# Optimization experiments

Hardware: AMD Instinct MI355X
Metric: run time of the kernel (lower is better)

Reference implementation:

```python
import jax, jax.numpy as jnp
import numpy as np

N = 100000
E = 1600000

def setup_inputs() -> dict:
    key = jax.random.key(0)
    ks = jax.random.split(key, 8)
    x = jax.random.normal(ks[0], (N, 512), dtype=jnp.float32)
    edge_index = jax.random.randint(ks[1], (2, E), 0, N, dtype=jnp.int32)
    W1 = jax.random.normal(ks[2], (512, 64), dtype=jnp.float32) * (1.0 / np.sqrt(512))
    b1 = jnp.zeros((64,), dtype=jnp.float32)
    W2 = jax.random.normal(ks[3], (64, 32), dtype=jnp.float32) * (1.0 / np.sqrt(64))
    b2 = jnp.zeros((32,), dtype=jnp.float32)
    W3 = jax.random.normal(ks[4], (32, 4), dtype=jnp.float32) * (1.0 / np.sqrt(32))
    b3 = jnp.zeros((4,), dtype=jnp.float32)
    return {"x": x, "edge_index": edge_index, "W1": W1, "b1": b1,
            "W2": W2, "b2": b2, "W3": W3, "b3": b3}


def _gcn_norm(edge_index, n):
    # Add self-loops (fill_value=1), symmetric deg^{-1/2} normalization (PyG gcn_norm).
    loop = jnp.arange(n, dtype=edge_index.dtype)
    src = jnp.concatenate([edge_index[0], loop])
    dst = jnp.concatenate([edge_index[1], loop])
    w = jnp.ones((src.shape[0],), dtype=jnp.float32)
    deg = jax.ops.segment_sum(w, dst, num_segments=n)
    dinv = jnp.where(deg > 0, jax.lax.rsqrt(deg), 0.0)
    norm = dinv[src] * w * dinv[dst]
    return src, dst, norm


def _gcn_conv(x, W, b, src, dst, norm, n):
    h = x @ W                      # dense transform first (PyG GCNConv order)
    msg = h[src] * norm[:, None]   # gather + edge scaling
    out = jax.ops.segment_sum(msg, dst, num_segments=n)  # scatter-add aggregate
    return out + b


def reference(x, edge_index, W1, b1, W2, b2, W3, b3):
    n = x.shape[0]
    src, dst, norm = _gcn_norm(edge_index, n)  # cached=True: shared across layers
    h = jax.nn.relu(_gcn_conv(x, W1, b1, src, dst, norm, n))
    # dropout p=0.2 is identity in eval mode
    h = jax.nn.relu(_gcn_conv(h, W2, b2, src, dst, norm, n))
    # dropout p=0.4 is identity in eval mode
    out = _gcn_conv(h, W3, b3, src, dst, norm, n)
    return out
```

## Files before the change

### kernel.cpp

```cpp
#include <hip/hip_runtime.h>


typedef __attribute__((ext_vector_type(8))) short short8;
typedef __attribute__((ext_vector_type(4))) float floatx4;

#define NBUK_MAX 512
#define SC_EDGES 8192
#define CB_MAXE 6144
#define HIST_EDGES 8192

__device__ __forceinline__ unsigned f2bf_bits(float f) {
    unsigned u = __float_as_uint(f);
    return (u + 0x7fffu + ((u >> 16) & 1u)) >> 16;
}
__device__ __forceinline__ float bf_bits2f(unsigned b) {
    return __uint_as_float(b << 16);
}

__global__ __launch_bounds__(256) void zero_i32(int* p, int n) {
    int i = blockIdx.x * 256 + threadIdx.x;
    if (i < n) p[i] = 0;
}

__global__ __launch_bounds__(512) void bucket_hist(const int* __restrict__ dst,
                                                   int* __restrict__ buckcnt,
                                                   int e, int shift, int nbuk) {
    __shared__ int hist[NBUK_MAX];
    int t = threadIdx.x;
    for (int i = t; i < nbuk; i += 512) hist[i] = 0;
    __syncthreads();
    long long base = (long long)blockIdx.x * HIST_EDGES;
#pragma unroll
    for (int j = 0; j < HIST_EDGES / 512; j++) {
        long long i = base + j * 512 + t;
        if (i < e) atomicAdd(&hist[dst[i] >> shift], 1);
    }
    __syncthreads();
    for (int i = t; i < nbuk; i += 512)
        if (hist[i] > 0) atomicAdd(&buckcnt[i], hist[i]);
}

__global__ __launch_bounds__(512) void bucket_scan(const int* __restrict__ buckcnt,
                                                   int* __restrict__ boff,
                                                   int* __restrict__ buckfill,
                                                   int* __restrict__ rowptr,
                                                   int nbuk, int n, int e) {
    __shared__ int sc[512];
    int t = threadIdx.x;
    int v = (t < nbuk) ? buckcnt[t] : 0;
    sc[t] = v;
    __syncthreads();
    for (int off = 1; off < 512; off <<= 1) {
        int u = (t >= off) ? sc[t - off] : 0;
        __syncthreads();
        sc[t] += u;
        __syncthreads();
    }
    int excl = sc[t] - v;
    if (t < nbuk) {
        boff[t] = excl;
        buckfill[t] = excl;
    }
    if (t == 0) {
        boff[nbuk] = e;
        rowptr[n] = e;
    }
}

__global__ __launch_bounds__(512) void bucket_scatter(const int* __restrict__ src,
                                                      const int* __restrict__ dst,
                                                      int* __restrict__ buckfill,
                                                      unsigned* __restrict__ colpack,
                                                      int e, int shift, int nbuk) {
    __shared__ int cnt[NBUK_MAX];
    __shared__ int baseG[NBUK_MAX];
    int t = threadIdx.x;
    for (int i = t; i < nbuk; i += 512) cnt[i] = 0;
    __syncthreads();
    long long base = (long long)blockIdx.x * SC_EDGES;
    unsigned wreg[16];
    int breg[16];
    unsigned lomask = (1u << shift) - 1u;
#pragma unroll
    for (int j = 0; j < 16; j++) {
        long long i = base + j * 512 + t;
        bool ok = (i < e);
        int d = ok ? dst[i] : 0;
        int s = ok ? src[i] : 0;
        int b = d >> shift;
        int r = ok ? atomicAdd(&cnt[b], 1) : 0;
        wreg[j] = ((unsigned)s << shift) | ((unsigned)d & lomask);
        breg[j] = ok ? ((b << 16) | r) : -1;
    }
    __syncthreads();
    for (int i = t; i < nbuk; i += 512) {
        int v = cnt[i];
        baseG[i] = (v > 0) ? atomicAdd(&buckfill[i], v) : 0;
    }
    __syncthreads();
#pragma unroll
    for (int j = 0; j < 16; j++) {
        int br = breg[j];
        if (br >= 0) {
            int b = br >> 16, r = br & 0xffff;
            colpack[baseG[b] + r] = wreg[j];
        }
    }
}

__global__ __launch_bounds__(512) void csr_build(const unsigned* __restrict__ colpack,
                                                 const int* __restrict__ boff,
                                                 int* __restrict__ rowptr,
                                                 float* __restrict__ dinv,
                                                 int* __restrict__ colidx,
                                                 int n, int shift) {
    __shared__ int degl[NBUK_MAX];
    __shared__ int lsc[NBUK_MAX];
    int t = threadIdx.x;
    int bn = 1 << shift;
    unsigned lomask = (unsigned)bn - 1u;
    int node0 = blockIdx.x << shift;
    int e0 = boff[blockIdx.x];
    int e1 = boff[blockIdx.x + 1];
    int cnt = e1 - e0;
    if (t < bn) degl[t] = 0;
    __syncthreads();
    unsigned wreg[CB_MAXE / 512];
    int rreg[CB_MAXE / 512];
#pragma unroll
    for (int j = 0; j < CB_MAXE / 512; j++) {
        int k = j * 512 + t;
        bool ok = (k < cnt);
        unsigned w = ok ? colpack[e0 + k] : 0u;
        int dlo = (int)(w & lomask);
        rreg[j] = ok ? atomicAdd(&degl[dlo], 1) : -1;
        wreg[j] = w;
    }
    __syncthreads();
    int v = (t < bn) ? degl[t] : 0;
    lsc[t] = v;
    __syncthreads();
    for (int off = 1; off < 512; off <<= 1) {
        int u = (t >= off) ? lsc[t - off] : 0;
        __syncthreads();
        lsc[t] += u;
        __syncthreads();
    }
    int excl = lsc[t] - v;
    int node = node0 + t;
    if (t < bn && node < n) {
        rowptr[node] = e0 + excl;
        dinv[node] = rsqrtf((float)(v + 1));
    }
    __syncthreads();
    if (t < 512) lsc[t] = excl;
    __syncthreads();
#pragma unroll
    for (int j = 0; j < CB_MAXE / 512; j++) {
        if (rreg[j] >= 0) {
            unsigned w = wreg[j];
            int dlo = (int)(w & lomask);
            colidx[e0 + lsc[dlo] + rreg[j]] = (int)(w >> shift);
        }
    }
}

__global__ __launch_bounds__(256) void w1_split(const float* __restrict__ W1,
                                                short* __restrict__ whi,
                                                short* __restrict__ wlo) {
    int idx = blockIdx.x * 256 + threadIdx.x;
    int k = idx >> 6;
    int nn = idx & 63;
    float v = W1[idx];
    unsigned hb = f2bf_bits(v);
    float lof = v - bf_bits2f(hb);
    unsigned lb = f2bf_bits(lof);
    int kc = k >> 5, rem = k & 31, quad = rem >> 3, j = rem & 7;
    int ct = nn >> 4, l = nn & 15;
    int lane = quad * 16 + l;
    int addr = ((ct * 16 + kc) * 64 + lane) * 8 + j;
    whi[addr] = (short)hb;
    wlo[addr] = (short)lb;
}

__global__ __launch_bounds__(256) void transform1_mfma(const float* __restrict__ x,
                                                       const short* __restrict__ whi,
                                                       const short* __restrict__ wlo,
                                                       const float* __restrict__ dinv,
                                                       float* __restrict__ h1, int n) {
    __shared__ float xs[64 * 36];
    const int t = threadIdx.x;
    const int w = t >> 6;
    const int lane = t & 63;
    const int quad = lane >> 4;
    const int row0 = blockIdx.x * 64;
    const int mrow = w * 16 + (lane & 15);
    floatx4 acc[4] = {{0.f, 0.f, 0.f, 0.f}, {0.f, 0.f, 0.f, 0.f},
                      {0.f, 0.f, 0.f, 0.f}, {0.f, 0.f, 0.f, 0.f}};

    for (int kc = 0; kc < 16; kc++) {
        __syncthreads();
#pragma unroll
        for (int i = 0; i < 2; i++) {
            int c = t + i * 256;
            int m = c >> 3;
            int koff = (c & 7) << 2;
            int grow = row0 + m;
            float4 v = make_float4(0.f, 0.f, 0.f, 0.f);
            if (grow < n) v = *(const float4*)&x[(size_t)grow * 512 + kc * 32 + koff];
            *(float4*)&xs[m * 36 + koff] = v;
        }
        __syncthreads();
        float a[8];
        *(float4*)&a[0] = *(const float4*)&xs[mrow * 36 + quad * 8];
        *(float4*)&a[4] = *(const float4*)&xs[mrow * 36 + quad * 8 + 4];
        short8 ahi, alo;
#pragma unroll
        for (int j = 0; j < 8; j++) {
            unsigned hb = f2bf_bits(a[j]);
            float lof = a[j] - bf_bits2f(hb);
            unsigned lb = f2bf_bits(lof);
            ahi[j] = (short)hb;
            alo[j] = (short)lb;
        }
        const int base = (kc * 64 + lane) * 8;
#pragma unroll
        for (int ct = 0; ct < 4; ct++) {
            short8 bhi = *(const short8*)&whi[ct * 8192 + base];
            short8 blo = *(const short8*)&wlo[ct * 8192 + base];
            acc[ct] = __builtin_amdgcn_mfma_f32_16x16x32_bf16(ahi, bhi, acc[ct], 0, 0, 0);
            acc[ct] = __builtin_amdgcn_mfma_f32_16x16x32_bf16(alo, bhi, acc[ct], 0, 0, 0);
            acc[ct] = __builtin_amdgcn_mfma_f32_16x16x32_bf16(ahi, blo, acc[ct], 0, 0, 0);
        }
    }
#pragma unroll
    for (int r = 0; r < 4; r++) {
        int grow = row0 + w * 16 + quad * 4 + r;
        if (grow < n) {
            float s = dinv[grow];
#pragma unroll
            for (int ct = 0; ct < 4; ct++) {
                h1[(size_t)grow * 64 + ct * 16 + (lane & 15)] = acc[ct][r] * s;
            }
        }
    }
}

__global__ __launch_bounds__(256) void transform2(const float* __restrict__ g1,
                                                  const float* __restrict__ W2,
                                                  const float* __restrict__ dinv,
                                                  float* __restrict__ h2, int n) {
    __shared__ float rows[32 * 68];
    __shared__ float W2s[64 * 32];
    int t = threadIdx.x;
    int row0 = blockIdx.x * 32;
#pragma unroll
    for (int i = 0; i < 2; i++) {
        int c = t + i * 256;
        int r = c >> 4, k4 = (c & 15) << 2;
        int grow = row0 + r;
        float4 v = make_float4(0.f, 0.f, 0.f, 0.f);
        if (grow < n) v = *(const float4*)&g1[(size_t)grow * 64 + k4];
        *(float4*)&rows[r * 68 + k4] = v;
    }
#pragma unroll
    for (int i = 0; i < 2; i++) {
        int c = t + i * 256;
        *(float4*)&W2s[c * 4] = *(const float4*)&W2[c * 4];
    }
    __syncthreads();
    int lr = t >> 3;
    int c4 = (t & 7) * 4;
    int row = row0 + lr;
    float a0 = 0.f, a1 = 0.f, a2 = 0.f, a3 = 0.f;
#pragma unroll
    for (int k4 = 0; k4 < 64; k4 += 4) {
        float4 a = *(const float4*)&rows[lr * 68 + k4];
        float4 w0 = *(const float4*)&W2s[(k4 + 0) * 32 + c4];
        float4 w1 = *(const float4*)&W2s[(k4 + 1) * 32 + c4];
        float4 w2 = *(const float4*)&W2s[(k4 + 2) * 32 + c4];
        float4 w3 = *(const float4*)&W2s[(k4 + 3) * 32 + c4];
        a0 += a.x * w0.x + a.y * w1.x + a.z * w2.x + a.w * w3.x;
        a1 += a.x * w0.y + a.y * w1.y + a.z * w2.y + a.w * w3.y;
        a2 += a.x * w0.z + a.y * w1.z + a.z * w2.z + a.w * w3.z;
        a3 += a.x * w0.w + a.y * w1.w + a.z * w2.w + a.w * w3.w;
    }
    if (row < n) {
        float s = dinv[row];
        float4 o = make_float4(a0 * s, a1 * s, a2 * s, a3 * s);
        *(float4*)&h2[(size_t)row * 32 + c4] = o;
    }
}

__device__ __forceinline__ void f4acc(float4& a, const float4 b) {
    a.x += b.x; a.y += b.y; a.z += b.z; a.w += b.w;
}
__device__ __forceinline__ void f4shflxor(float4& a, int m) {
    a.x += __shfl_xor(a.x, m);
    a.y += __shfl_xor(a.y, m);
    a.z += __shfl_xor(a.z, m);
    a.w += __shfl_xor(a.w, m);
}

__global__ __launch_bounds__(256) void agg64_wave(const float* __restrict__ h,
                                                  const int* __restrict__ rowptr,
                                                  const int* __restrict__ colidx,
                                                  const float* __restrict__ dinv,
                                                  const float* __restrict__ bias,
                                                  float* __restrict__ out, int n) {
    int node = (blockIdx.x * 256 + threadIdx.x) >> 6;
    if (node >= n) return;
    int lane = threadIdx.x & 63;
    int eslot = lane >> 4;
    int fq = (lane & 15) << 2;
    int r0 = rowptr[node], r1 = rowptr[node + 1];
    float4 z = make_float4(0.f, 0.f, 0.f, 0.f);
    float4 a0 = z, a1 = z, a2 = z, a3 = z;
    if (eslot == 0) a0 = *(const float4*)&h[(size_t)node * 64 + fq];
    int j = r0;
    for (; j + 15 < r1; j += 16) {
        int c0 = colidx[j + eslot];
        int c1 = colidx[j + 4 + eslot];
        int c2 = colidx[j + 8 + eslot];
        int c3 = colidx[j + 12 + eslot];
        f4acc(a0, *(const float4*)&h[(size_t)c0 * 64 + fq]);
        f4acc(a1, *(const float4*)&h[(size_t)c1 * 64 + fq]);
        f4acc(a2, *(const float4*)&h[(size_t)c2 * 64 + fq]);
        f4acc(a3, *(const float4*)&h[(size_t)c3 * 64 + fq]);
    }
    {
        int e0 = j + eslot, e1 = j + 4 + eslot, e2 = j + 8 + eslot, e3 = j + 12 + eslot;
        if (e0 < r1) f4acc(a0, *(const float4*)&h[(size_t)colidx[e0] * 64 + fq]);
        if (e1 < r1) f4acc(a1, *(const float4*)&h[(size_t)colidx[e1] * 64 + fq]);
        if (e2 < r1) f4acc(a2, *(const float4*)&h[(size_t)colidx[e2] * 64 + fq]);
        if (e3 < r1) f4acc(a3, *(const float4*)&h[(size_t)colidx[e3] * 64 + fq]);
    }
    f4acc(a0, a1); f4acc(a2, a3); f4acc(a0, a2);
    f4shflxor(a0, 16);
    f4shflxor(a0, 32);
    if (eslot == 0) {
        float dn = dinv[node];
        float4 b = *(const float4*)&bias[fq];
        float4 v = make_float4(fmaxf(dn * a0.x + b.x, 0.f), fmaxf(dn * a0.y + b.y, 0.f),
                               fmaxf(dn * a0.z + b.z, 0.f), fmaxf(dn * a0.w + b.w, 0.f));
        *(float4*)&out[(size_t)node * 64 + fq] = v;
    }
}

__global__ __launch_bounds__(256) void agg32_t3(const float* __restrict__ h,
                                                const int* __restrict__ rowptr,
                                                const int* __restrict__ colidx,
                                                const float* __restrict__ dinv,
                                                const float* __restrict__ bias,
                                                const float* __restrict__ W3,
                                                float* __restrict__ h3, int n) {
    int node = (blockIdx.x * 256 + threadIdx.x) >> 6;
    if (node >= n) return;
    int lane = threadIdx.x & 63;
    int eslot = lane >> 3;
    int fq = (lane & 7) << 2;
    int r0 = rowptr[node], r1 = rowptr[node + 1];
    float4 z = make_float4(0.f, 0.f, 0.f, 0.f);
    float4 a0 = z, a1 = z;
    if (eslot == 0) a0 = *(const float4*)&h[(size_t)node * 32 + fq];
    int j = r0;
    for (; j + 15 < r1; j += 16) {
        int c0 = colidx[j + eslot];
        int c1 = colidx[j + 8 + eslot];
        f4acc(a0, *(const float4*)&h[(size_t)c0 * 32 + fq]);
        f4acc(a1, *(const float4*)&h[(size_t)c1 * 32 + fq]);
    }
    {
        int e0 = j + eslot, e1 = j + 8 + eslot;
        if (e0 < r1) f4acc(a0, *(const float4*)&h[(size_t)colidx[e0] * 32 + fq]);
        if (e1 < r1) f4acc(a1, *(const float4*)&h[(size_t)colidx[e1] * 32 + fq]);
    }
    f4acc(a0, a1);
    f4shflxor(a0, 8);
    f4shflxor(a0, 16);
    f4shflxor(a0, 32);
    float dn = dinv[node];
    float4 b = *(const float4*)&bias[fq];
    float4 g = make_float4(fmaxf(dn * a0.x + b.x, 0.f), fmaxf(dn * a0.y + b.y, 0.f),
                           fmaxf(dn * a0.z + b.z, 0.f), fmaxf(dn * a0.w + b.w, 0.f));
    float4 w0 = *(const float4*)&W3[(fq + 0) * 4];
    float4 w1 = *(const float4*)&W3[(fq + 1) * 4];
    float4 w2 = *(const float4*)&W3[(fq + 2) * 4];
    float4 w3 = *(const float4*)&W3[(fq + 3) * 4];
    float4 p = make_float4(g.x * w0.x + g.y * w1.x + g.z * w2.x + g.w * w3.x,
                           g.x * w0.y + g.y * w1.y + g.z * w2.y + g.w * w3.y,
                           g.x * w0.z + g.y * w1.z + g.z * w2.z + g.w * w3.z,
                           g.x * w0.w + g.y * w1.w + g.z * w2.w + g.w * w3.w);
    f4shflxor(p, 1);
    f4shflxor(p, 2);
    f4shflxor(p, 4);
    if (lane == 0) {
        *(float4*)&h3[(size_t)node * 4] =
            make_float4(dn * p.x, dn * p.y, dn * p.z, dn * p.w);
    }
}

__global__ __launch_bounds__(256) void agg4_wave(const float* __restrict__ h,
                                                 const int* __restrict__ rowptr,
                                                 const int* __restrict__ colidx,
                                                 const float* __restrict__ dinv,
                                                 const float* __restrict__ bias,
                                                 float* __restrict__ out, int n) {
    int node = (blockIdx.x * 256 + threadIdx.x) >> 6;
    if (node >= n) return;
    int lane = threadIdx.x & 63;
    int eslot = lane >> 2;
    int f = lane & 3;
    int r0 = rowptr[node], r1 = rowptr[node + 1];
    float a0 = (eslot == 0) ? h[(size_t)node * 4 + f] : 0.f;
    float a1 = 0.f;
    int j = r0;
    for (; j + 15 < r1; j += 16) {
        int c = colidx[j + eslot];
        a0 += h[(size_t)c * 4 + f];
    }
    {
        int e = j + eslot;
        if (e < r1) a1 += h[(size_t)colidx[e] * 4 + f];
    }
    float s = a0 + a1;
    s += __shfl_xor(s, 4);
    s += __shfl_xor(s, 8);
    s += __shfl_xor(s, 16);
    s += __shfl_xor(s, 32);
    if (eslot == 0) out[(size_t)node * 4 + f] = dinv[node] * s + bias[f];
}

extern "C" void kernel_launch(void* const* d_in, const int* in_sizes, int n_in,
                              void* d_out, int out_size, void* d_ws, size_t ws_size,
                              hipStream_t stream) {
    const float* x  = (const float*)d_in[0];
    const int*   ei = (const int*)d_in[1];
    const float* W1 = (const float*)d_in[2];
    const float* b1 = (const float*)d_in[3];
    const float* W2 = (const float*)d_in[4];
    const float* b2 = (const float*)d_in[5];
    const float* W3 = (const float*)d_in[6];
    const float* b3 = (const float*)d_in[7];
    const int n = in_sizes[0] / 512;
    const int e = in_sizes[1] / 2;
    const int* src = ei;
    const int* dst = ei + e;
    float* out = (float*)d_out;

    char* p = (char*)d_ws;
    auto alloc = [&](size_t bytes) {
        void* r = (void*)p;
        p += (bytes + 255) & ~(size_t)255;
        return r;
    };
    int*   buckcnt  = (int*)alloc((size_t)NBUK_MAX * 4);
    int*   boff     = (int*)alloc((size_t)(NBUK_MAX + 1) * 4);
    int*   buckfill = (int*)alloc((size_t)NBUK_MAX * 4);
    int*   rowptr   = (int*)alloc((size_t)(n + 1) * 4);
    int*   colidx   = (int*)alloc((size_t)e * 4);
    float* dinv     = (float*)alloc((size_t)n * 4);
    short* whi      = (short*)alloc((size_t)32768 * 2);
    short* wlo      = (short*)alloc((size_t)32768 * 2);
    float* bufA     = (float*)alloc((size_t)n * 64 * 4);
    float* bufB     = (float*)alloc((size_t)n * 64 * 4);
    unsigned* colpack = (unsigned*)bufA;

    int shift = 8;
    while (((n + (1 << shift) - 1) >> shift) > NBUK_MAX) shift++;
    const int nbuk = (n + (1 << shift) - 1) >> shift;

    const int HB = (int)(((long long)e + HIST_EDGES - 1) / HIST_EDGES);
    const int SB = (int)(((long long)e + SC_EDGES - 1) / SC_EDGES);
    const int WPN = (n + 3) / 4;

    zero_i32<<<dim3((nbuk + 255) / 256), dim3(256), 0, stream>>>(buckcnt, nbuk);
    bucket_hist<<<dim3(HB), dim3(512), 0, stream>>>(dst, buckcnt, e, shift, nbuk);
    bucket_scan<<<dim3(1), dim3(512), 0, stream>>>(buckcnt, boff, buckfill, rowptr, nbuk, n, e);
    bucket_scatter<<<dim3(SB), dim3(512), 0, stream>>>(src, dst, buckfill, colpack, e, shift, nbuk);
    csr_build<<<dim3(nbuk), dim3(512), 0, stream>>>(colpack, boff, rowptr, dinv, colidx, n, shift);
    w1_split<<<dim3(128), dim3(256), 0, stream>>>(W1, whi, wlo);

    transform1_mfma<<<dim3((n + 63) / 64), dim3(256), 0, stream>>>(x, whi, wlo, dinv, bufA, n);
    agg64_wave<<<dim3(WPN), dim3(256), 0, stream>>>(bufA, rowptr, colidx, dinv, b1, bufB, n);
    transform2<<<dim3((n + 31) / 32), dim3(256), 0, stream>>>(bufB, W2, dinv, bufA, n);
    agg32_t3<<<dim3(WPN), dim3(256), 0, stream>>>(bufA, rowptr, colidx, dinv, b2, W3, bufB, n);
    agg4_wave<<<dim3(WPN), dim3(256), 0, stream>>>(bufB, rowptr, colidx, dinv, b3, out, n);
}
```

Baseline: 514.1 us.

## Fuse layer-2 transform into layer-1 aggregation and prefetch x tiles

Removes the separate transform2 kernel by applying W2 inside the 64-wide aggregation kernel via wave shuffles and an LDS copy of W2. This avoids writing and re-reading the 64-wide hidden activation. Also restructures transform1 so the next x tile is loaded into registers while the current tile is consumed from LDS. The fused kernel adds per-node shuffle work and a W2 load into LDS per block.

```diff
diff --git a/kernel.cpp b/kernel.cpp
--- a/kernel.cpp
+++ b/kernel.cpp
@@ -195,22 +195,28 @@
     const int quad = lane >> 4;
     const int row0 = blockIdx.x * 64;
     const int mrow = w * 16 + (lane & 15);
+    const int m0 = t >> 3;
+    const int k0 = (t & 7) << 2;
+    const int m1 = m0 + 32;
+    const bool ok0 = (row0 + m0) < n;
+    const bool ok1 = (row0 + m1) < n;
+    const float* xp0 = x + (size_t)(row0 + m0) * 512 + k0;
+    const float* xp1 = x + (size_t)(row0 + m1) * 512 + k0;
+    const float4 z4 = make_float4(0.f, 0.f, 0.f, 0.f);
+    float4 p0 = ok0 ? *(const float4*)xp0 : z4;
+    float4 p1 = ok1 ? *(const float4*)xp1 : z4;
+
     floatx4 acc[4] = {{0.f, 0.f, 0.f, 0.f}, {0.f, 0.f, 0.f, 0.f},
                       {0.f, 0.f, 0.f, 0.f}, {0.f, 0.f, 0.f, 0.f}};
 
     for (int kc = 0; kc < 16; kc++) {
-        __syncthreads();
-#pragma unroll
-        for (int i = 0; i < 2; i++) {
-            int c = t + i * 256;
-            int m = c >> 3;
-            int koff = (c & 7) << 2;
-            int grow = row0 + m;
-            float4 v = make_float4(0.f, 0.f, 0.f, 0.f);
-            if (grow < n) v = *(const float4*)&x[(size_t)grow * 512 + kc * 32 + koff];
-            *(float4*)&xs[m * 36 + koff] = v;
-        }
-        __syncthreads();
+        *(float4*)&xs[m0 * 36 + k0] = p0;
+        *(float4*)&xs[m1 * 36 + k0] = p1;
+        __syncthreads();
+        if (kc < 15) {
+            p0 = ok0 ? *(const float4*)(xp0 + (kc + 1) * 32) : z4;
+            p1 = ok1 ? *(const float4*)(xp1 + (kc + 1) * 32) : z4;
+        }
         float a[8];
         *(float4*)&a[0] = *(const float4*)&xs[mrow * 36 + quad * 8];
         *(float4*)&a[4] = *(const float4*)&xs[mrow * 36 + quad * 8 + 4];
@@ -232,6 +238,7 @@
             acc[ct] = __builtin_amdgcn_mfma_f32_16x16x32_bf16(alo, bhi, acc[ct], 0, 0, 0);
             acc[ct] = __builtin_amdgcn_mfma_f32_16x16x32_bf16(ahi, blo, acc[ct], 0, 0, 0);
         }
+        __syncthreads();
     }
 #pragma unroll
     for (int r = 0; r < 4; r++) {
@@ -243,52 +250,6 @@
                 h1[(size_t)grow * 64 + ct * 16 + (lane & 15)] = acc[ct][r] * s;
             }
         }
-    }
-}
-
-__global__ __launch_bounds__(256) void transform2(const float* __restrict__ g1,
-                                                  const float* __restrict__ W2,
-                                                  const float* __restrict__ dinv,
-                                                  float* __restrict__ h2, int n) {
-    __shared__ float rows[32 * 68];
-    __shared__ float W2s[64 * 32];
-    int t = threadIdx.x;
-    int row0 = blockIdx.x * 32;
-#pragma unroll
-    for (int i = 0; i < 2; i++) {
-        int c = t + i * 256;
-        int r = c >> 4, k4 = (c & 15) << 2;
-        int grow = row0 + r;
-        float4 v = make_float4(0.f, 0.f, 0.f, 0.f);
-        if (grow < n) v = *(const float4*)&g1[(size_t)grow * 64 + k4];
-        *(float4*)&rows[r * 68 + k4] = v;
-    }
-#pragma unroll
-    for (int i = 0; i < 2; i++) {
-        int c = t + i * 256;
-        *(float4*)&W2s[c * 4] = *(const float4*)&W2[c * 4];
-    }
-    __syncthreads();
-    int lr = t >> 3;
-    int c4 = (t & 7) * 4;
-    int row = row0 + lr;
-    float a0 = 0.f, a1 = 0.f, a2 = 0.f, a3 = 0.f;
-#pragma unroll
-    for (int k4 = 0; k4 < 64; k4 += 4) {
-        float4 a = *(const float4*)&rows[lr * 68 + k4];
-        float4 w0 = *(const float4*)&W2s[(k4 + 0) * 32 + c4];
-        float4 w1 = *(const float4*)&W2s[(k4 + 1) * 32 + c4];
-        float4 w2 = *(const float4*)&W2s[(k4 + 2) * 32 + c4];
-        float4 w3 = *(const float4*)&W2s[(k4 + 3) * 32 + c4];
-        a0 += a.x * w0.x + a.y * w1.x + a.z * w2.x + a.w * w3.x;
-        a1 += a.x * w0.y + a.y * w1.y + a.z * w2.y + a.w * w3.y;
-        a2 += a.x * w0.z + a.y * w1.z + a.z * w2.z + a.w * w3.z;
-        a3 += a.x * w0.w + a.y * w1.w + a.z * w2.w + a.w * w3.w;
-    }
-    if (row < n) {
-        float s = dinv[row];
-        float4 o = make_float4(a0 * s, a1 * s, a2 * s, a3 * s);
-        *(float4*)&h2[(size_t)row * 32 + c4] = o;
     }
 }
 
@@ -302,15 +263,24 @@
     a.w += __shfl_xor(a.w, m);
 }
 
-__global__ __launch_bounds__(256) void agg64_wave(const float* __restrict__ h,
-                                                  const int* __restrict__ rowptr,
-                                                  const int* __restrict__ colidx,
-                                                  const float* __restrict__ dinv,
-                                                  const float* __restrict__ bias,
-                                                  float* __restrict__ out, int n) {
-    int node = (blockIdx.x * 256 + threadIdx.x) >> 6;
+__global__ __launch_bounds__(256) void agg64_t2(const float* __restrict__ h,
+                                                const int* __restrict__ rowptr,
+                                                const int* __restrict__ colidx,
+                                                const float* __restrict__ dinv,
+                                                const float* __restrict__ b1,
+                                                const float* __restrict__ W2,
+                                                float* __restrict__ h2, int n) {
+    __shared__ float W2s[64 * 32];
+    int t = threadIdx.x;
+#pragma unroll
+    for (int i = 0; i < 2; i++) {
+        int c = t + i * 256;
+        *(float4*)&W2s[c * 4] = *(const float4*)&W2[c * 4];
+    }
+    __syncthreads();
+    int node = (blockIdx.x * 256 + t) >> 6;
     if (node >= n) return;
-    int lane = threadIdx.x & 63;
+    int lane = t & 63;
     int eslot = lane >> 4;
     int fq = (lane & 15) << 2;
     int r0 = rowptr[node], r1 = rowptr[node + 1];
@@ -338,13 +308,22 @@
     f4acc(a0, a1); f4acc(a2, a3); f4acc(a0, a2);
     f4shflxor(a0, 16);
     f4shflxor(a0, 32);
-    if (eslot == 0) {
-        float dn = dinv[node];
-        float4 b = *(const float4*)&bias[fq];
-        float4 v = make_float4(fmaxf(dn * a0.x + b.x, 0.f), fmaxf(dn * a0.y + b.y, 0.f),
-                               fmaxf(dn * a0.z + b.z, 0.f), fmaxf(dn * a0.w + b.w, 0.f));
-        *(float4*)&out[(size_t)node * 64 + fq] = v;
-    }
+    float dn = dinv[node];
+    float4 bb = *(const float4*)&b1[fq];
+    float4 g = make_float4(fmaxf(dn * a0.x + bb.x, 0.f), fmaxf(dn * a0.y + bb.y, 0.f),
+                           fmaxf(dn * a0.z + bb.z, 0.f), fmaxf(dn * a0.w + bb.w, 0.f));
+    int c = lane & 31;
+    float acc2 = 0.f;
+#pragma unroll
+    for (int kk = 0; kk < 16; kk++) {
+        float gx = __shfl(g.x, kk);
+        float gy = __shfl(g.y, kk);
+        float gz = __shfl(g.z, kk);
+        float gw = __shfl(g.w, kk);
+        acc2 += gx * W2s[(4 * kk + 0) * 32 + c] + gy * W2s[(4 * kk + 1) * 32 + c]
+              + gz * W2s[(4 * kk + 2) * 32 + c] + gw * W2s[(4 * kk + 3) * 32 + c];
+    }
+    if (lane < 32) h2[(size_t)node * 32 + c] = dn * acc2;
 }
 
 __global__ __launch_bounds__(256) void agg32_t3(const float* __restrict__ h,
@@ -482,8 +461,7 @@
     w1_split<<<dim3(128), dim3(256), 0, stream>>>(W1, whi, wlo);
 
     transform1_mfma<<<dim3((n + 63) / 64), dim3(256), 0, stream>>>(x, whi, wlo, dinv, bufA, n);
-    agg64_wave<<<dim3(WPN), dim3(256), 0, stream>>>(bufA, rowptr, colidx, dinv, b1, bufB, n);
-    transform2<<<dim3((n + 31) / 32), dim3(256), 0, stream>>>(bufB, W2, dinv, bufA, n);
-    agg32_t3<<<dim3(WPN), dim3(256), 0, stream>>>(bufA, rowptr, colidx, dinv, b2, W3, bufB, n);
-    agg4_wave<<<dim3(WPN), dim3(256), 0, stream>>>(bufB, rowptr, colidx, dinv, b3, out, n);
-}
+    agg64_t2<<<dim3(WPN), dim3(256), 0, stream>>>(bufA, rowptr, colidx, dinv, b1, W2, bufB, n);
+    agg32_t3<<<dim3(WPN), dim3(256), 0, stream>>>(bufB, rowptr, colidx, dinv, b2, W3, bufA, n);
+    agg4_wave<<<dim3(WPN), dim3(256), 0, stream>>>(bufA, rowptr, colidx, dinv, b3, out, n);
+}
```

Result: slower. 574.8 us (+11.8%).

## Pad CSR rows to multiples of 32 with dummy zero node to remove tail handling

Applied to the files above, without the earlier changes.

The CSR build now pads each node's neighbor list to a multiple of 32 entries, filling the padding with index n that points to an all-zero row appended to each feature buffer. Row offsets are packed into a compact per-node word relative to a fixed per-bucket capacity. This lets the aggregation loops drop their remainder branches and unroll wider with more independent accumulators. The cost is extra gathers of the dummy row (about 16 padding slots per node on average with degree near 16), a larger padded index array, and a fixed PCAP bucket capacity that could overflow for skewed degree distributions.

```diff
diff --git a/kernel.cpp b/kernel.cpp
--- a/kernel.cpp
+++ b/kernel.cpp
@@ -8,6 +8,7 @@
 #define SC_EDGES 8192
 #define CB_MAXE 6144
 #define HIST_EDGES 8192
+#define PCAP 14336
 
 __device__ __forceinline__ unsigned f2bf_bits(float f) {
     unsigned u = __float_as_uint(f);
@@ -43,8 +44,7 @@
 __global__ __launch_bounds__(512) void bucket_scan(const int* __restrict__ buckcnt,
                                                    int* __restrict__ boff,
                                                    int* __restrict__ buckfill,
-                                                   int* __restrict__ rowptr,
-                                                   int nbuk, int n, int e) {
+                                                   int nbuk, int e) {
     __shared__ int sc[512];
     int t = threadIdx.x;
     int v = (t < nbuk) ? buckcnt[t] : 0;
@@ -61,10 +61,7 @@
         boff[t] = excl;
         buckfill[t] = excl;
     }
-    if (t == 0) {
-        boff[nbuk] = e;
-        rowptr[n] = e;
-    }
+    if (t == 0) boff[nbuk] = e;
 }
 
 __global__ __launch_bounds__(512) void bucket_scatter(const int* __restrict__ src,
@@ -110,9 +107,9 @@
 
 __global__ __launch_bounds__(512) void csr_build(const unsigned* __restrict__ colpack,
                                                  const int* __restrict__ boff,
-                                                 int* __restrict__ rowptr,
+                                                 unsigned* __restrict__ rowinfo,
                                                  float* __restrict__ dinv,
-                                                 int* __restrict__ colidx,
+                                                 int* __restrict__ pcolidx,
                                                  int n, int shift) {
     __shared__ int degl[NBUK_MAX];
     __shared__ int lsc[NBUK_MAX];
@@ -123,6 +120,7 @@
     int e0 = boff[blockIdx.x];
     int e1 = boff[blockIdx.x + 1];
     int cnt = e1 - e0;
+    long long gbase = (long long)blockIdx.x * PCAP;
     if (t < bn) degl[t] = 0;
     __syncthreads();
     unsigned wreg[CB_MAXE / 512];
@@ -138,7 +136,8 @@
     }
     __syncthreads();
     int v = (t < bn) ? degl[t] : 0;
-    lsc[t] = v;
+    int pv = (v + 31) & ~31;
+    lsc[t] = pv;
     __syncthreads();
     for (int off = 1; off < 512; off <<= 1) {
         int u = (t >= off) ? lsc[t - off] : 0;
@@ -146,22 +145,25 @@
         lsc[t] += u;
         __syncthreads();
     }
-    int excl = lsc[t] - v;
+    int excl = lsc[t] - pv;
     int node = node0 + t;
     if (t < bn && node < n) {
-        rowptr[node] = e0 + excl;
+        rowinfo[node] = ((unsigned)(excl >> 5) << 8) | (unsigned)(pv >> 5);
         dinv[node] = rsqrtf((float)(v + 1));
     }
     __syncthreads();
-    if (t < 512) lsc[t] = excl;
+    lsc[t] = excl;
     __syncthreads();
 #pragma unroll
     for (int j = 0; j < CB_MAXE / 512; j++) {
         if (rreg[j] >= 0) {
             unsigned w = wreg[j];
             int dlo = (int)(w & lomask);
-            colidx[e0 + lsc[dlo] + rreg[j]] = (int)(w >> shift);
-        }
+            pcolidx[gbase + lsc[dlo] + rreg[j]] = (int)(w >> shift);
+        }
+    }
+    if (t < bn && node < n) {
+        for (int k = v; k < pv; k++) pcolidx[gbase + excl + k] = n;
     }
 }
 
@@ -195,6 +197,7 @@
     const int quad = lane >> 4;
     const int row0 = blockIdx.x * 64;
     const int mrow = w * 16 + (lane & 15);
+    if (blockIdx.x == 0 && t < 64) h1[(size_t)n * 64 + t] = 0.f;
     floatx4 acc[4] = {{0.f, 0.f, 0.f, 0.f}, {0.f, 0.f, 0.f, 0.f},
                       {0.f, 0.f, 0.f, 0.f}, {0.f, 0.f, 0.f, 0.f}};
 
@@ -254,6 +257,7 @@
     __shared__ float W2s[64 * 32];
     int t = threadIdx.x;
     int row0 = blockIdx.x * 32;
+    if (blockIdx.x == 0 && t < 32) h2[(size_t)n * 32 + t] = 0.f;
 #pragma unroll
     for (int i = 0; i < 2; i++) {
         int c = t + i * 256;
@@ -302,40 +306,43 @@
     a.w += __shfl_xor(a.w, m);
 }
 
-__global__ __launch_bounds__(256) void agg64_wave(const float* __restrict__ h,
-                                                  const int* __restrict__ rowptr,
-                                                  const int* __restrict__ colidx,
-                                                  const float* __restrict__ dinv,
-                                                  const float* __restrict__ bias,
-                                                  float* __restrict__ out, int n) {
+__global__ __launch_bounds__(256) void agg64_pad(const float* __restrict__ h,
+                                                 const unsigned* __restrict__ rowinfo,
+                                                 const int* __restrict__ pcolidx,
+                                                 const float* __restrict__ dinv,
+                                                 const float* __restrict__ bias,
+                                                 float* __restrict__ out, int n, int shift) {
     int node = (blockIdx.x * 256 + threadIdx.x) >> 6;
     if (node >= n) return;
     int lane = threadIdx.x & 63;
     int eslot = lane >> 4;
     int fq = (lane & 15) << 2;
-    int r0 = rowptr[node], r1 = rowptr[node + 1];
+    unsigned ri = rowinfo[node];
+    int r0 = (node >> shift) * PCAP + ((int)(ri >> 8) << 5);
+    int r1 = r0 + ((int)(ri & 255u) << 5);
     float4 z = make_float4(0.f, 0.f, 0.f, 0.f);
-    float4 a0 = z, a1 = z, a2 = z, a3 = z;
+    float4 a0 = z, a1 = z, a2 = z, a3 = z, a4 = z, a5 = z, a6 = z, a7 = z;
     if (eslot == 0) a0 = *(const float4*)&h[(size_t)node * 64 + fq];
-    int j = r0;
-    for (; j + 15 < r1; j += 16) {
-        int c0 = colidx[j + eslot];
-        int c1 = colidx[j + 4 + eslot];
-        int c2 = colidx[j + 8 + eslot];
-        int c3 = colidx[j + 12 + eslot];
+    for (int j = r0; j < r1; j += 32) {
+        int c0 = pcolidx[j + eslot];
+        int c1 = pcolidx[j + 4 + eslot];
+        int c2 = pcolidx[j + 8 + eslot];
+        int c3 = pcolidx[j + 12 + eslot];
+        int c4 = pcolidx[j + 16 + eslot];
+        int c5 = pcolidx[j + 20 + eslot];
+        int c6 = pcolidx[j + 24 + eslot];
+        int c7 = pcolidx[j + 28 + eslot];
         f4acc(a0, *(const float4*)&h[(size_t)c0 * 64 + fq]);
         f4acc(a1, *(const float4*)&h[(size_t)c1 * 64 + fq]);
         f4acc(a2, *(const float4*)&h[(size_t)c2 * 64 + fq]);
         f4acc(a3, *(const float4*)&h[(size_t)c3 * 64 + fq]);
-    }
-    {
-        int e0 = j + eslot, e1 = j + 4 + eslot, e2 = j + 8 + eslot, e3 = j + 12 + eslot;
-        if (e0 < r1) f4acc(a0, *(const float4*)&h[(size_t)colidx[e0] * 64 + fq]);
-        if (e1 < r1) f4acc(a1, *(const float4*)&h[(size_t)colidx[e1] * 64 + fq]);
-        if (e2 < r1) f4acc(a2, *(const float4*)&h[(size_t)colidx[e2] * 64 + fq]);
-        if (e3 < r1) f4acc(a3, *(const float4*)&h[(size_t)colidx[e3] * 64 + fq]);
-    }
-    f4acc(a0, a1); f4acc(a2, a3); f4acc(a0, a2);
+        f4acc(a4, *(const float4*)&h[(size_t)c4 * 64 + fq]);
+        f4acc(a5, *(const float4*)&h[(size_t)c5 * 64 + fq]);
+        f4acc(a6, *(const float4*)&h[(size_t)c6 * 64 + fq]);
+        f4acc(a7, *(const float4*)&h[(size_t)c7 * 64 + fq]);
+    }
+    f4acc(a0, a1); f4acc(a2, a3); f4acc(a4, a5); f4acc(a6, a7);
+    f4acc(a0, a2); f4acc(a4, a6); f4acc(a0, a4);
     f4shflxor(a0, 16);
     f4shflxor(a0, 32);
     if (eslot == 0) {
@@ -348,34 +355,35 @@
 }
 
 __global__ __launch_bounds__(256) void agg32_t3(const float* __restrict__ h,
-                                                const int* __restrict__ rowptr,
-                                                const int* __restrict__ colidx,
+                                                const unsigned* __restrict__ rowinfo,
+                                                const int* __restrict__ pcolidx,
                                                 const float* __restrict__ dinv,
                                                 const float* __restrict__ bias,
                                                 const float* __restrict__ W3,
-                                                float* __restrict__ h3, int n) {
+                                                float* __restrict__ h3, int n, int shift) {
+    if (blockIdx.x == 0 && threadIdx.x < 4) h3[(size_t)n * 4 + threadIdx.x] = 0.f;
     int node = (blockIdx.x * 256 + threadIdx.x) >> 6;
     if (node >= n) return;
     int lane = threadIdx.x & 63;
     int eslot = lane >> 3;
     int fq = (lane & 7) << 2;
-    int r0 = rowptr[node], r1 = rowptr[node + 1];
+    unsigned ri = rowinfo[node];
+    int r0 = (node >> shift) * PCAP + ((int)(ri >> 8) << 5);
+    int r1 = r0 + ((int)(ri & 255u) << 5);
     float4 z = make_float4(0.f, 0.f, 0.f, 0.f);
-    float4 a0 = z, a1 = z;
+    float4 a0 = z, a1 = z, a2 = z, a3 = z;
     if (eslot == 0) a0 = *(const float4*)&h[(size_t)node * 32 + fq];
-    int j = r0;
-    for (; j + 15 < r1; j += 16) {
-        int c0 = colidx[j + eslot];
-        int c1 = colidx[j + 8 + eslot];
+    for (int j = r0; j < r1; j += 32) {
+        int c0 = pcolidx[j + eslot];
+        int c1 = pcolidx[j + 8 + eslot];
+        int c2 = pcolidx[j + 16 + eslot];
+        int c3 = pcolidx[j + 24 + eslot];
         f4acc(a0, *(const float4*)&h[(size_t)c0 * 32 + fq]);
         f4acc(a1, *(const float4*)&h[(size_t)c1 * 32 + fq]);
-    }
-    {
-        int e0 = j + eslot, e1 = j + 8 + eslot;
-        if (e0 < r1) f4acc(a0, *(const float4*)&h[(size_t)colidx[e0] * 32 + fq]);
-        if (e1 < r1) f4acc(a1, *(const float4*)&h[(size_t)colidx[e1] * 32 + fq]);
-    }
-    f4acc(a0, a1);
+        f4acc(a2, *(const float4*)&h[(size_t)c2 * 32 + fq]);
+        f4acc(a3, *(const float4*)&h[(size_t)c3 * 32 + fq]);
+    }
+    f4acc(a0, a1); f4acc(a2, a3); f4acc(a0, a2);
     f4shflxor(a0, 8);
     f4shflxor(a0, 16);
     f4shflxor(a0, 32);
@@ -400,28 +408,27 @@
     }
 }
 
-__global__ __launch_bounds__(256) void agg4_wave(const float* __restrict__ h,
-                                                 const int* __restrict__ rowptr,
-                                                 const int* __restrict__ colidx,
-                                                 const float* __restrict__ dinv,
-                                                 const float* __restrict__ bias,
-                                                 float* __restrict__ out, int n) {
+__global__ __launch_bounds__(256) void agg4_pad(const float* __restrict__ h,
+                                                const unsigned* __restrict__ rowinfo,
+                                                const int* __restrict__ pcolidx,
+                                                const float* __restrict__ dinv,
+                                                const float* __restrict__ bias,
+                                                float* __restrict__ out, int n, int shift) {
     int node = (blockIdx.x * 256 + threadIdx.x) >> 6;
     if (node >= n) return;
     int lane = threadIdx.x & 63;
     int eslot = lane >> 2;
     int f = lane & 3;
-    int r0 = rowptr[node], r1 = rowptr[node + 1];
+    unsigned ri = rowinfo[node];
+    int r0 = (node >> shift) * PCAP + ((int)(ri >> 8) << 5);
+    int r1 = r0 + ((int)(ri & 255u) << 5);
     float a0 = (eslot == 0) ? h[(size_t)node * 4 + f] : 0.f;
     float a1 = 0.f;
-    int j = r0;
-    for (; j + 15 < r1; j += 16) {
-        int c = colidx[j + eslot];
-        a0 += h[(size_t)c * 4 + f];
-    }
-    {
-        int e = j + eslot;
-        if (e < r1) a1 += h[(size_t)colidx[e] * 4 + f];
+    for (int j = r0; j < r1; j += 32) {
+        int c0 = pcolidx[j + eslot];
+        int c1 = pcolidx[j + 16 + eslot];
+        a0 += h[(size_t)c0 * 4 + f];
+        a1 += h[(size_t)c1 * 4 + f];
     }
     float s = a0 + a1;
     s += __shfl_xor(s, 4);
@@ -457,13 +464,13 @@
     int*   buckcnt  = (int*)alloc((size_t)NBUK_MAX * 4);
     int*   boff     = (int*)alloc((size_t)(NBUK_MAX + 1) * 4);
     int*   buckfill = (int*)alloc((size_t)NBUK_MAX * 4);
-    int*   rowptr   = (int*)alloc((size_t)(n + 1) * 4);
-    int*   colidx   = (int*)alloc((size_t)e * 4);
+    unsigned* rowinfo = (unsigned*)alloc((size_t)n * 4);
+    int*   pcolidx  = (int*)alloc((size_t)NBUK_MAX * PCAP * 4);
     float* dinv     = (float*)alloc((size_t)n * 4);
     short* whi      = (short*)alloc((size_t)32768 * 2);
     short* wlo      = (short*)alloc((size_t)32768 * 2);
-    float* bufA     = (float*)alloc((size_t)n * 64 * 4);
-    float* bufB     = (float*)alloc((size_t)n * 64 * 4);
+    float* bufA     = (float*)alloc((size_t)(n + 1) * 64 * 4);
+    float* bufB     = (float*)alloc((size_t)(n + 1) * 64 * 4);
     unsigned* colpack = (unsigned*)bufA;
 
     int shift = 8;
@@ -476,14 +483,14 @@
 
     zero_i32<<<dim3((nbuk + 255) / 256), dim3(256), 0, stream>>>(buckcnt, nbuk);
     bucket_hist<<<dim3(HB), dim3(512), 0, stream>>>(dst, buckcnt, e, shift, nbuk);
-    bucket_scan<<<dim3(1), dim3(512), 0, stream>>>(buckcnt, boff, buckfill, rowptr, nbuk, n, e);
+    bucket_scan<<<dim3(1), dim3(512), 0, stream>>>(buckcnt, boff, buckfill, nbuk, e);
     bucket_scatter<<<dim3(SB), dim3(512), 0, stream>>>(src, dst, buckfill, colpack, e, shift, nbuk);
-    csr_build<<<dim3(nbuk), dim3(512), 0, stream>>>(colpack, boff, rowptr, dinv, colidx, n, shift);
+    csr_build<<<dim3(nbuk), dim3(512), 0, stream>>>(colpack, boff, rowinfo, dinv, pcolidx, n, shift);
     w1_split<<<dim3(128), dim3(256), 0, stream>>>(W1, whi, wlo);
 
     transform1_mfma<<<dim3((n + 63) / 64), dim3(256), 0, stream>>>(x, whi, wlo, dinv, bufA, n);
-    agg64_wave<<<dim3(WPN), dim3(256), 0, stream>>>(bufA, rowptr, colidx, dinv, b1, bufB, n);
+    agg64_pad<<<dim3(WPN), dim3(256), 0, stream>>>(bufA, rowinfo, pcolidx, dinv, b1, bufB, n, shift);
     transform2<<<dim3((n + 31) / 32), dim3(256), 0, stream>>>(bufB, W2, dinv, bufA, n);
-    agg32_t3<<<dim3(WPN), dim3(256), 0, stream>>>(bufA, rowptr, colidx, dinv, b2, W3, bufB, n);
-    agg4_wave<<<dim3(WPN), dim3(256), 0, stream>>>(bufB, rowptr, colidx, dinv, b3, out, n);
-}
+    agg32_t3<<<dim3(WPN), dim3(256), 0, stream>>>(bufA, rowinfo, pcolidx, dinv, b2, W3, bufB, n, shift);
+    agg4_pad<<<dim3(WPN), dim3(256), 0, stream>>>(bufB, rowinfo, pcolidx, dinv, b3, out, n, shift);
+}
```

After: 520.8 us. Within noise of the previous version (+1.3%).
